# Kernel optimization log

Hardware: AMD Instinct MI355X
Metric: run time of the kernel (lower is better)

## Reference

```python
import jax, jax.numpy as jnp
import numpy as np
from jax import lax

B, C_IN, H, W = 4, 256, 64, 64
C_OUT = 512
KEY_DIM = C_OUT // 2   # 256
VAL_DIM = C_OUT // 2   # 256
HEADS = 8
EPS = 1e-5


def _conv(x, w, stride, pad):
    return lax.conv_general_dilated(
        x, w, (stride, stride), [(pad, pad), (pad, pad)],
        dimension_numbers=('NCHW', 'OIHW', 'NCHW'))


def setup_inputs() -> dict:
    key = jax.random.key(0)
    ks = jax.random.split(key, 10)
    x = jax.random.normal(ks[0], (B, C_IN, H, W), jnp.float32)
    bn_gamma = jax.random.uniform(ks[1], (C_IN,), jnp.float32, 0.5, 1.5)
    bn_beta = jax.random.normal(ks[2], (C_IN,), jnp.float32) * 0.1
    bn_mean = jax.random.normal(ks[3], (C_IN,), jnp.float32) * 0.1
    bn_var = jax.random.uniform(ks[4], (C_IN,), jnp.float32, 0.5, 1.5)
    w_short = jax.random.normal(ks[5], (C_OUT, C_IN, 3, 3), jnp.float32) * (1.0 / np.sqrt(C_IN * 9))
    wq = jax.random.normal(ks[6], (KEY_DIM, C_IN, 1, 1), jnp.float32) * (1.0 / np.sqrt(C_IN))
    wk = jax.random.normal(ks[7], (KEY_DIM, C_IN, 1, 1), jnp.float32) * (1.0 / np.sqrt(C_IN))
    wv = jax.random.normal(ks[8], (VAL_DIM, C_IN, 1, 1), jnp.float32) * (1.0 / np.sqrt(C_IN))
    wo = jax.random.normal(ks[9], (C_OUT, VAL_DIM, 1, 1), jnp.float32) * (1.0 / np.sqrt(VAL_DIM))
    return dict(x=x, bn_gamma=bn_gamma, bn_beta=bn_beta, bn_mean=bn_mean,
                bn_var=bn_var, w_short=w_short, wq=wq, wk=wk, wv=wv, wo=wo)


def reference(x, bn_gamma, bn_beta, bn_mean, bn_var, w_short, wq, wk, wv, wo):
    # BatchNorm (inference: running stats) + ReLU, fused elementwise chain
    inv = bn_gamma / jnp.sqrt(bn_var + EPS)
    h = jax.nn.relu((x - bn_mean[None, :, None, None]) * inv[None, :, None, None]
                    + bn_beta[None, :, None, None])

    # Projection shortcut: 3x3 conv, stride 2, pad 1, no bias -> [B, C_OUT, H/2, W/2]
    shortcut = _conv(h, w_short, 2, 1)

    # DOWN attention: queries at stride 2 (downsampled grid), keys/values at full res
    q = _conv(h, wq, 2, 0)   # [B, KEY_DIM, H/2, W/2]
    k = _conv(h, wk, 1, 0)   # [B, KEY_DIM, H, W]
    v = _conv(h, wv, 1, 0)   # [B, VAL_DIM, H, W]

    Ho, Wo = H // 2, W // 2
    dk = KEY_DIM // HEADS
    dv = VAL_DIM // HEADS
    Nq, Nk = Ho * Wo, H * W

    qh = q.reshape(B, HEADS, dk, Nq)
    kh = k.reshape(B, HEADS, dk, Nk)
    vh = v.reshape(B, HEADS, dv, Nk)

    scale = 1.0 / np.sqrt(dk)
    scores = jnp.einsum('bhdq,bhdk->bhqk', qh, kh) * scale  # [B,H,Nq,Nk]
    attn = jax.nn.softmax(scores, axis=-1)                  # use_softmax=True
    out = jnp.einsum('bhqk,bhdk->bhdq', attn, vh)           # [B,H,dv,Nq]
    out = out.reshape(B, VAL_DIM, Ho, Wo)
    out = _conv(out, wo, 1, 0)                              # [B, C_OUT, Ho, Wo]

    return shortcut + out
```

## Files before the change

### kernel.cpp

```cpp
#include <hip/hip_runtime.h>

#define BB    4
#define CIN   256
#define NPIX  4096
#define COUT  512
#define KD    256
#define HEADS 8
#define NQ    1024
#define NK    4096
#define EPSV  1e-5f
#define QSCALE (0.17677669529663687f * 1.4426950408889634f)

using short8 = __attribute__((ext_vector_type(8))) short;
using f32x4  = __attribute__((ext_vector_type(4))) float;

__device__ __forceinline__ float b2f(unsigned u){ return __uint_as_float(u << 16); }
__device__ __forceinline__ unsigned short f2b(float f){
  unsigned u = __float_as_uint(f);
  return (unsigned short)((u + 0x7fffu + ((u >> 16) & 1u)) >> 16);
}
__device__ __forceinline__ float bnrelu(float xv, float inv, float mu, float bt){
  return fmaxf((xv - mu) * inv + bt, 0.0f);
}
__device__ __forceinline__ unsigned pkbf(float lo, float hi){
  unsigned a = __float_as_uint(lo) + 0x8000u;
  unsigned b = __float_as_uint(hi) + 0x8000u;
  return __builtin_amdgcn_perm(b, a, 0x07060302u);
}
__device__ __forceinline__ unsigned cvtpk(float lo, float hi){
  unsigned r;
  asm("v_cvt_pk_bf16_f32 %0, %1, %2" : "=v"(r) : "v"(lo), "v"(hi));
  return r;
}

__global__ __launch_bounds__(256) void prep_h(
    const float* __restrict__ x, const float* __restrict__ gam,
    const float* __restrict__ bet, const float* __restrict__ mea,
    const float* __restrict__ var, unsigned short* __restrict__ h_t){
  __shared__ unsigned short T[64][264];
  const int b = blockIdx.y;
  const int pix0 = blockIdx.x * 64;
  const int t = threadIdx.x;
  const int w = t >> 6, lane = t & 63;
  for (int cc = 0; cc < 32; ++cc){
    int c0 = cc * 8 + w * 2;
    float i0 = gam[c0]   * rsqrtf(var[c0]   + EPSV), mu0 = mea[c0],   bt0 = bet[c0];
    float i1 = gam[c0+1] * rsqrtf(var[c0+1] + EPSV), mu1 = mea[c0+1], bt1 = bet[c0+1];
    float v0 = bnrelu(x[((size_t)(b*CIN + c0  ))*NPIX + pix0 + lane], i0, mu0, bt0);
    float v1 = bnrelu(x[((size_t)(b*CIN + c0+1))*NPIX + pix0 + lane], i1, mu1, bt1);
    *(unsigned*)&T[lane][c0] = pkbf(v0, v1);
  }
  __syncthreads();
  int p = t >> 2;
  unsigned short* dst = h_t + ((size_t)b * NPIX + pix0 + p) * CIN;
  #pragma unroll
  for (int i = 0; i < 8; ++i){
    int coff = i * 32 + (t & 3) * 8;
    *(uint4*)(dst + coff) = *(const uint4*)&T[p][coff];
  }
}

#define WF_K  2560
#define WF_E  (512*2560)
__global__ __launch_bounds__(256) void prep_w3(
    const float* __restrict__ wsh, const float* __restrict__ wq,
    const float* __restrict__ wk,  const float* __restrict__ wv,
    const float* __restrict__ wo,  unsigned short* __restrict__ W2){
  const int blk = blockIdx.x;
  const int t = threadIdx.x;
  if (blk < 512){
    __shared__ float R[2304];
    const float* src = wsh + (size_t)blk * 2304;
    #pragma unroll
    for (int i = 0; i < 9; ++i) R[i * 256 + t] = src[i * 256 + t];
    __syncthreads();
    unsigned short* dst = W2 + (size_t)blk * WF_K;
    #pragma unroll
    for (int i = 0; i < 9; ++i){
      int kp = i * 256 + t;
      int tap = kp >> 8, ci = kp & 255;
      dst[kp] = f2b(R[ci * 9 + tap]);
    }
  } else if (blk < 704){
    int idx = (blk - 512) * 1024 + t * 4;
    float4 v;
    if (idx < 65536){
      v = *(const float4*)(wq + idx);
      v.x *= QSCALE; v.y *= QSCALE; v.z *= QSCALE; v.w *= QSCALE;
    } else if (idx < 2*65536){ v = *(const float4*)(wk + idx - 65536);
    } else {                   v = *(const float4*)(wv + idx - 2*65536); }
    uint2 pk;
    pk.x = (unsigned)f2b(v.x) | ((unsigned)f2b(v.y) << 16);
    pk.y = (unsigned)f2b(v.z) | ((unsigned)f2b(v.w) << 16);
    *(uint2*)(W2 + WF_E + idx) = pk;
  } else {
    int idx = (blk - 704) * 1024 + t * 4;
    int m = idx >> 8, c = idx & 255;
    float4 v = *(const float4*)(wo + idx);
    uint2 pk;
    pk.x = (unsigned)f2b(v.x) | ((unsigned)f2b(v.y) << 16);
    pk.y = (unsigned)f2b(v.z) | ((unsigned)f2b(v.w) << 16);
    *(uint2*)(W2 + (size_t)m * WF_K + 2304 + c) = pk;
  }
}

__global__ __launch_bounds__(256) void kv_gemm(
    const unsigned short* __restrict__ Wkv,
    const unsigned short* __restrict__ h_t,
    unsigned short* __restrict__ ktg,
    unsigned short* __restrict__ vtg){
  const int b  = blockIdx.z;
  const int m0 = blockIdx.y * 64;
  const bool isv = m0 >= 256;
  const int n0 = blockIdx.x * 128;
  const int t  = threadIdx.x;
  const int w = t >> 6, lane = t & 63, col = lane & 15, quad = lane >> 4;
  const int wm = w & 1, wn = w >> 1;
  __shared__ unsigned short As[64][40];
  __shared__ unsigned short Bs[128][40];
  f32x4 acc[2][4];
  #pragma unroll
  for (int i = 0; i < 2; ++i)
    #pragma unroll
    for (int j = 0; j < 4; ++j) acc[i][j] = (f32x4){0.f,0.f,0.f,0.f};
  const int am = t >> 2, ak = (t & 3) * 8;
  const int bn = t >> 1, bkh = (t & 1) * 16;
  const size_t browbase = ((size_t)b * NPIX + (n0 + bn)) * CIN;

  uint4 av  = *(const uint4*)(Wkv + (size_t)(m0 + am) * 256 + ak);
  uint4 bv0 = *(const uint4*)(h_t + browbase + bkh);
  uint4 bv1 = *(const uint4*)(h_t + browbase + bkh + 8);

  for (int k0 = 0; k0 < 256; k0 += 32){
    *(uint4*)&As[am][ak]      = av;
    *(uint4*)&Bs[bn][bkh]     = bv0;
    *(uint4*)&Bs[bn][bkh + 8] = bv1;
    __syncthreads();
    if (k0 + 32 < 256){
      av  = *(const uint4*)(Wkv + (size_t)(m0 + am) * 256 + k0 + 32 + ak);
      bv0 = *(const uint4*)(h_t + browbase + k0 + 32 + bkh);
      bv1 = *(const uint4*)(h_t + browbase + k0 + 32 + bkh + 8);
    }
    short8 af[2], bf[4];
    af[0] = *(const short8*)&As[wm * 32 +      col][quad * 8];
    af[1] = *(const short8*)&As[wm * 32 + 16 + col][quad * 8];
    #pragma unroll
    for (int j = 0; j < 4; ++j)
      bf[j] = *(const short8*)&Bs[wn * 64 + j * 16 + col][quad * 8];
    if (!isv){
      #pragma unroll
      for (int i = 0; i < 2; ++i)
        #pragma unroll
        for (int j = 0; j < 4; ++j)
          acc[i][j] = __builtin_amdgcn_mfma_f32_16x16x32_bf16(af[i], bf[j], acc[i][j], 0, 0, 0);
    } else {
      #pragma unroll
      for (int i = 0; i < 2; ++i)
        #pragma unroll
        for (int j = 0; j < 4; ++j)
          acc[i][j] = __builtin_amdgcn_mfma_f32_16x16x32_bf16(bf[j], af[i], acc[i][j], 0, 0, 0);
    }
    __syncthreads();
  }

  if (!isv){
    int head = (m0 + wm * 32) >> 5;
    #pragma unroll
    for (int i = 0; i < 2; ++i){
      int d0 = i * 16 + quad * 4;
      #pragma unroll
      for (int j = 0; j < 4; ++j){
        int n = n0 + wn * 64 + j * 16 + col;
        uint2 pk;
        pk.x = pkbf(acc[i][j][0], acc[i][j][1]);
        pk.y = pkbf(acc[i][j][2], acc[i][j][3]);
        *(uint2*)(ktg + ((size_t)(b * HEADS + head) * NK + n) * 32 + d0) = pk;
      }
    }
  } else {
    int head = ((m0 - 256) + wm * 32) >> 5;
    #pragma unroll
    for (int i = 0; i < 2; ++i){
      int d = i * 16 + col;
      #pragma unroll
      for (int j = 0; j < 4; ++j){
        int nb = n0 + wn * 64 + j * 16 + quad * 4;
        size_t addr = (((size_t)(b * HEADS + head) * 128 + (nb >> 5)) * 32 + d) * 32 + (nb & 31);
        uint2 pk;
        pk.x = pkbf(acc[i][j][0], acc[i][j][1]);
        pk.y = pkbf(acc[i][j][2], acc[i][j][3]);
        *(uint2*)(vtg + addr) = pk;
      }
    }
  }
}

__global__ __launch_bounds__(256) void q_gemm(
    const unsigned short* __restrict__ Wq,
    const unsigned short* __restrict__ h_t,
    unsigned short* __restrict__ qt){
  const int b  = blockIdx.z;
  const int m0 = blockIdx.y * 64;
  const int n0 = blockIdx.x * 64;
  const int t  = threadIdx.x;
  const int w = t >> 6, lane = t & 63, col = lane & 15, quad = lane >> 4;
  const int wm = w & 1, wn = w >> 1;
  __shared__ unsigned short As[64][40];
  __shared__ unsigned short Bs[64][40];
  f32x4 acc[2][2];
  #pragma unroll
  for (int i = 0; i < 2; ++i)
    #pragma unroll
    for (int j = 0; j < 2; ++j) acc[i][j] = (f32x4){0.f,0.f,0.f,0.f};
  const int am = t >> 2, ak = (t & 3) * 8;
  const int bn = t >> 2, bk = (t & 3) * 8;
  int n = n0 + bn;
  const size_t browbase = ((size_t)b * NPIX + (((n >> 5) << 7) + ((n & 31) << 1))) * CIN;

  uint4 av = *(const uint4*)(Wq + (size_t)(m0 + am) * 256 + ak);
  uint4 bv = *(const uint4*)(h_t + browbase + bk);

  for (int k0 = 0; k0 < 256; k0 += 32){
    *(uint4*)&As[am][ak] = av;
    *(uint4*)&Bs[bn][bk] = bv;
    __syncthreads();
    if (k0 + 32 < 256){
      av = *(const uint4*)(Wq + (size_t)(m0 + am) * 256 + k0 + 32 + ak);
      bv = *(const uint4*)(h_t + browbase + k0 + 32 + bk);
    }
    short8 af[2], bf[2];
    af[0] = *(const short8*)&As[wm * 32 +      col][quad * 8];
    af[1] = *(const short8*)&As[wm * 32 + 16 + col][quad * 8];
    bf[0] = *(const short8*)&Bs[wn * 32 +      col][quad * 8];
    bf[1] = *(const short8*)&Bs[wn * 32 + 16 + col][quad * 8];
    #pragma unroll
    for (int i = 0; i < 2; ++i)
      #pragma unroll
      for (int j = 0; j < 2; ++j)
        acc[i][j] = __builtin_amdgcn_mfma_f32_16x16x32_bf16(af[i], bf[j], acc[i][j], 0, 0, 0);
    __syncthreads();
  }

  int head = (m0 + wm * 32) >> 5;
  #pragma unroll
  for (int i = 0; i < 2; ++i){
    int d0 = i * 16 + quad * 4;
    #pragma unroll
    for (int j = 0; j < 2; ++j){
      int nn = n0 + wn * 32 + j * 16 + col;
      uint2 pk;
      pk.x = pkbf(acc[i][j][0], acc[i][j][1]);
      pk.y = pkbf(acc[i][j][2], acc[i][j][3]);
      *(uint2*)(qt + ((size_t)(b * HEADS + head) * NQ + nn) * 32 + d0) = pk;
    }
  }
}

__global__ __launch_bounds__(256) void scwo_gemm(
    const unsigned short* __restrict__ Wf,
    const unsigned short* __restrict__ h_t,
    const unsigned short* __restrict__ aot,
    float* __restrict__ outf){
  const int b  = blockIdx.z;
  const int m0 = blockIdx.y * 64;
  const int n0 = blockIdx.x * 64;
  const int t  = threadIdx.x;
  const int w = t >> 6, lane = t & 63, col = lane & 15, quad = lane >> 4;
  const int wm = w & 1, wn = w >> 1;
  __shared__ unsigned short As[64][40];
  __shared__ unsigned short Bs[64][40];
  f32x4 acc[2][2];
  #pragma unroll
  for (int i = 0; i < 2; ++i)
    #pragma unroll
    for (int j = 0; j < 2; ++j) acc[i][j] = (f32x4){0.f,0.f,0.f,0.f};
  const int am = t >> 2, ak = (t & 3) * 8;
  const int bn = t >> 2, bk = (t & 3) * 8;
  const int n = n0 + bn;
  const int oy = n >> 5, ox = n & 31;
  const size_t aobase = ((size_t)b * NQ + n) * KD;

  auto loadB = [&](int k0) -> uint4 {
    if (k0 < 2304){
      int tap = k0 >> 8;
      int ky = tap / 3, kx = tap - ky * 3;
      int iy = 2 * oy + ky - 1, ix = 2 * ox + kx - 1;
      if (((unsigned)iy < 64u) && ((unsigned)ix < 64u))
        return *(const uint4*)(h_t + ((size_t)b * NPIX + iy * 64 + ix) * CIN + (k0 & 255) + bk);
      return make_uint4(0,0,0,0);
    }
    return *(const uint4*)(aot + aobase + (k0 - 2304) + bk);
  };

  uint4 av = *(const uint4*)(Wf + (size_t)(m0 + am) * WF_K + ak);
  uint4 bv = loadB(0);

  for (int k0 = 0; k0 < WF_K; k0 += 32){
    *(uint4*)&As[am][ak] = av;
    *(uint4*)&Bs[bn][bk] = bv;
    __syncthreads();
    if (k0 + 32 < WF_K){
      av = *(const uint4*)(Wf + (size_t)(m0 + am) * WF_K + k0 + 32 + ak);
      bv = loadB(k0 + 32);
    }
    short8 af[2], bf[2];
    af[0] = *(const short8*)&As[wm * 32 +      col][quad * 8];
    af[1] = *(const short8*)&As[wm * 32 + 16 + col][quad * 8];
    bf[0] = *(const short8*)&Bs[wn * 32 +      col][quad * 8];
    bf[1] = *(const short8*)&Bs[wn * 32 + 16 + col][quad * 8];
    #pragma unroll
    for (int i = 0; i < 2; ++i)
      #pragma unroll
      for (int j = 0; j < 2; ++j)
        acc[i][j] = __builtin_amdgcn_mfma_f32_16x16x32_bf16(bf[j], af[i], acc[i][j], 0, 0, 0);
    __syncthreads();
  }

  #pragma unroll
  for (int i = 0; i < 2; ++i){
    int co = m0 + wm * 32 + i * 16 + col;
    #pragma unroll
    for (int j = 0; j < 2; ++j){
      int nb = n0 + wn * 32 + j * 16 + quad * 4;
      float4 o;
      o.x = acc[i][j][0]; o.y = acc[i][j][1];
      o.z = acc[i][j][2]; o.w = acc[i][j][3];
      *(float4*)(outf + ((size_t)(b * COUT + co)) * NQ + nb) = o;
    }
  }
}

__global__ __launch_bounds__(256) void attn8(
    const unsigned short* __restrict__ qt,
    const unsigned short* __restrict__ ktg,
    const unsigned short* __restrict__ vtg,
    unsigned short* __restrict__ aot){
  __shared__ float Om4[4][64][8];
  __shared__ float Ll4[4][64];
  const int bid = blockIdx.x;
  const int xcd = bid & 7, slot = bid >> 3;
  const int bh = xcd * 4 + (slot >> 6);
  const int qblk = slot & 63;
  const int b = bh >> 3, hd = bh & 7;
  const int t = threadIdx.x;
  const int w = t >> 6, lane = t & 63, col = lane & 15, quad = lane >> 4;
  const int q = qblk * 16 + col;

  short8 qf = *(const short8*)(qt + ((size_t)bh * NQ + q) * 32 + quad * 8);
  const unsigned short* kb = ktg + (size_t)bh * NK * 32;
  const unsigned short* vb = vtg + (size_t)bh * 128 * 1024;
  const int ks = w * 1024, ke = ks + 1024;

  short8 kf0 = *(const short8*)(kb + (size_t)(ks +      col) * 32 + quad * 8);
  short8 kf1 = *(const short8*)(kb + (size_t)(ks + 16 + col) * 32 + quad * 8);
  short8 vf0 = *(const short8*)(vb + ((ks >> 5) << 10) +       col * 32 + quad * 8);
  short8 vf1 = *(const short8*)(vb + ((ks >> 5) << 10) + 512 + col * 32 + quad * 8);

  f32x4 O0 = {0.f,0.f,0.f,0.f}, O1 = {0.f,0.f,0.f,0.f}, l4 = {0.f,0.f,0.f,0.f};
  const short8 ones = {0x3F80,0x3F80,0x3F80,0x3F80,0x3F80,0x3F80,0x3F80,0x3F80};

  for (int k0 = ks; k0 < ke; k0 += 32){
    int kn = (k0 + 32 < ke) ? (k0 + 32) : ks;
    int cn = (kn >> 5) << 10;
    short8 nk0 = *(const short8*)(kb + (size_t)(kn +      col) * 32 + quad * 8);
    short8 nk1 = *(const short8*)(kb + (size_t)(kn + 16 + col) * 32 + quad * 8);
    short8 nv0 = *(const short8*)(vb + cn +       col * 32 + quad * 8);
    short8 nv1 = *(const short8*)(vb + cn + 512 + col * 32 + quad * 8);

    f32x4 z = {0.f,0.f,0.f,0.f};
    f32x4 slo = __builtin_amdgcn_mfma_f32_16x16x32_bf16(kf0, qf, z, 0, 0, 0);
    f32x4 shi = __builtin_amdgcn_mfma_f32_16x16x32_bf16(kf1, qf, z, 0, 0, 0);

    unsigned x0 = cvtpk(__builtin_amdgcn_exp2f(slo[0]), __builtin_amdgcn_exp2f(slo[1]));
    unsigned x1 = cvtpk(__builtin_amdgcn_exp2f(slo[2]), __builtin_amdgcn_exp2f(slo[3]));
    unsigned y0 = cvtpk(__builtin_amdgcn_exp2f(shi[0]), __builtin_amdgcn_exp2f(shi[1]));
    unsigned y1 = cvtpk(__builtin_amdgcn_exp2f(shi[2]), __builtin_amdgcn_exp2f(shi[3]));

    asm("v_permlane32_swap_b32 %0, %1" : "+v"(x0), "+v"(y0));
    asm("v_permlane32_swap_b32 %0, %1" : "+v"(x1), "+v"(y1));
    asm("v_permlane16_swap_b32 %0, %1" : "+v"(x0), "+v"(y0));
    asm("v_permlane16_swap_b32 %0, %1" : "+v"(x1), "+v"(y1));
    unsigned f[4] = {x0, x1, y0, y1};
    short8 pf;
    memcpy(&pf, f, 16);

    O0 = __builtin_amdgcn_mfma_f32_16x16x32_bf16(vf0, pf, O0, 0, 0, 0);
    O1 = __builtin_amdgcn_mfma_f32_16x16x32_bf16(vf1, pf, O1, 0, 0, 0);
    l4 = __builtin_amdgcn_mfma_f32_16x16x32_bf16(ones, pf, l4, 0, 0, 0);
    kf0 = nk0; kf1 = nk1; vf0 = nv0; vf1 = nv1;
  }

  Ll4[w][lane] = l4[0];
  *(f32x4*)&Om4[w][lane][0] = O0;
  *(f32x4*)&Om4[w][lane][4] = O1;
  __syncthreads();
  if (w == 0){
    float L = l4[0] + Ll4[1][lane] + Ll4[2][lane] + Ll4[3][lane];
    float o[8];
    #pragma unroll
    for (int j = 0; j < 8; ++j)
      o[j] = Om4[0][lane][j] + Om4[1][lane][j] + Om4[2][lane][j] + Om4[3][lane][j];
    float inv = 1.0f / L;
    unsigned short* dst = aot + ((size_t)(b * NQ + q)) * KD + hd * 32;
    uint2 pk;
    pk.x = pkbf(o[0] * inv, o[1] * inv);
    pk.y = pkbf(o[2] * inv, o[3] * inv);
    *(uint2*)(dst + quad * 4) = pk;
    pk.x = pkbf(o[4] * inv, o[5] * inv);
    pk.y = pkbf(o[6] * inv, o[7] * inv);
    *(uint2*)(dst + 16 + quad * 4) = pk;
  }
}

extern "C" void kernel_launch(void* const* d_in, const int* in_sizes, int n_in,
                              void* d_out, int out_size, void* d_ws, size_t ws_size,
                              hipStream_t stream){
  const float* x   = (const float*)d_in[0];
  const float* bg  = (const float*)d_in[1];
  const float* bbt = (const float*)d_in[2];
  const float* bm  = (const float*)d_in[3];
  const float* bv  = (const float*)d_in[4];
  const float* wsh = (const float*)d_in[5];
  const float* wq  = (const float*)d_in[6];
  const float* wk  = (const float*)d_in[7];
  const float* wvv = (const float*)d_in[8];
  const float* wo  = (const float*)d_in[9];
  float* out = (float*)d_out;

  unsigned short* h_t = (unsigned short*)d_ws;
  unsigned short* W2  = h_t + (size_t)BB * NPIX * CIN;
  unsigned short* qt  = W2  + (WF_E + 3*65536);
  unsigned short* aot = qt  + (size_t)BB * HEADS * NQ * 32;
  unsigned short* ktg = aot + (size_t)BB * NQ * KD;
  unsigned short* vtg = ktg + (size_t)BB * HEADS * NK * 32;
  size_t need = ((size_t)(vtg + (size_t)BB * HEADS * 32 * NK - h_t)) * 2;
  if (ws_size < need) return;

  unsigned short* Wf   = W2;
  unsigned short* wq2  = W2 + WF_E;
  unsigned short* wkv2 = wq2 + 65536;

  prep_h<<<dim3(64, 4), dim3(256), 0, stream>>>(x, bg, bbt, bm, bv, h_t);
  prep_w3<<<dim3(832), dim3(256), 0, stream>>>(wsh, wq, wk, wvv, wo, W2);
  q_gemm<<<dim3(16, 4, 4), dim3(256), 0, stream>>>(wq2, h_t, qt);
  kv_gemm<<<dim3(32, 8, 4), dim3(256), 0, stream>>>(wkv2, h_t, ktg, vtg);
  attn8<<<dim3(2048), dim3(256), 0, stream>>>(qt, ktg, vtg, aot);
  scwo_gemm<<<dim3(16, 8, 4), dim3(256), 0, stream>>>(Wf, h_t, aot, out);
}
```

Baseline: 205.3 us.

## Share K/V tiles across query blocks via double-buffered LDS in attention

The attention kernel changes from four waves splitting the key range for one 16-query block, with an LDS reduction at the end, to eight waves each owning a different 16-query block. All eight waves iterate over the full key range, and K/V tiles are staged cooperatively into double-buffered shared memory. This cuts redundant global/L2 reads of K and V by sharing each tile across eight query blocks and removes the final cross-wave reduction. In exchange there is a block-wide barrier every iteration, only 256 blocks (one per CU), and a longer serial key loop per wave.

```diff
diff --git a/kernel.cpp b/kernel.cpp
--- a/kernel.cpp
+++ b/kernel.cpp
@@ -330,86 +330,88 @@
   }
 }
 
-__global__ __launch_bounds__(256) void attn8(
+__global__ __launch_bounds__(512) void attn9b(
     const unsigned short* __restrict__ qt,
     const unsigned short* __restrict__ ktg,
     const unsigned short* __restrict__ vtg,
     unsigned short* __restrict__ aot){
-  __shared__ float Om4[4][64][8];
-  __shared__ float Ll4[4][64];
+  __shared__ unsigned short KV[2][4096];
   const int bid = blockIdx.x;
-  const int xcd = bid & 7, slot = bid >> 3;
-  const int bh = xcd * 4 + (slot >> 6);
-  const int qblk = slot & 63;
+  const int xcd = bid & 7, idx = bid >> 3;
+  const int bh = xcd * 4 + (idx & 3);
+  const int qg = idx >> 2;
   const int b = bh >> 3, hd = bh & 7;
   const int t = threadIdx.x;
   const int w = t >> 6, lane = t & 63, col = lane & 15, quad = lane >> 4;
-  const int q = qblk * 16 + col;
+  const int q = (qg * 8 + w) * 16 + col;
 
   short8 qf = *(const short8*)(qt + ((size_t)bh * NQ + q) * 32 + quad * 8);
   const unsigned short* kb = ktg + (size_t)bh * NK * 32;
   const unsigned short* vb = vtg + (size_t)bh * 128 * 1024;
-  const int ks = w * 1024, ke = ks + 1024;
-
-  short8 kf0 = *(const short8*)(kb + (size_t)(ks +      col) * 32 + quad * 8);
-  short8 kf1 = *(const short8*)(kb + (size_t)(ks + 16 + col) * 32 + quad * 8);
-  short8 vf0 = *(const short8*)(vb + ((ks >> 5) << 10) +       col * 32 + quad * 8);
-  short8 vf1 = *(const short8*)(vb + ((ks >> 5) << 10) + 512 + col * 32 + quad * 8);
+
+  const int sg = (w & 3) >> 1, sf = w & 1;
+  const size_t ksrc = (size_t)(32 * sg + 16 * sf + col) * 32 + quad * 8;
+  const size_t vsrc = (size_t)sg * 1024 + (size_t)(16 * sf + col) * 32 + quad * 8;
+  unsigned short* dstp = &KV[0][w * 512 + lane * 8];
 
   f32x4 O0 = {0.f,0.f,0.f,0.f}, O1 = {0.f,0.f,0.f,0.f}, l4 = {0.f,0.f,0.f,0.f};
   const short8 ones = {0x3F80,0x3F80,0x3F80,0x3F80,0x3F80,0x3F80,0x3F80,0x3F80};
 
-  for (int k0 = ks; k0 < ke; k0 += 32){
-    int kn = (k0 + 32 < ke) ? (k0 + 32) : ks;
-    int cn = (kn >> 5) << 10;
-    short8 nk0 = *(const short8*)(kb + (size_t)(kn +      col) * 32 + quad * 8);
-    short8 nk1 = *(const short8*)(kb + (size_t)(kn + 16 + col) * 32 + quad * 8);
-    short8 nv0 = *(const short8*)(vb + cn +       col * 32 + quad * 8);
-    short8 nv1 = *(const short8*)(vb + cn + 512 + col * 32 + quad * 8);
-
-    f32x4 z = {0.f,0.f,0.f,0.f};
-    f32x4 slo = __builtin_amdgcn_mfma_f32_16x16x32_bf16(kf0, qf, z, 0, 0, 0);
-    f32x4 shi = __builtin_amdgcn_mfma_f32_16x16x32_bf16(kf1, qf, z, 0, 0, 0);
-
-    unsigned x0 = cvtpk(__builtin_amdgcn_exp2f(slo[0]), __builtin_amdgcn_exp2f(slo[1]));
-    unsigned x1 = cvtpk(__builtin_amdgcn_exp2f(slo[2]), __builtin_amdgcn_exp2f(slo[3]));
-    unsigned y0 = cvtpk(__builtin_amdgcn_exp2f(shi[0]), __builtin_amdgcn_exp2f(shi[1]));
-    unsigned y1 = cvtpk(__builtin_amdgcn_exp2f(shi[2]), __builtin_amdgcn_exp2f(shi[3]));
-
-    asm("v_permlane32_swap_b32 %0, %1" : "+v"(x0), "+v"(y0));
-    asm("v_permlane32_swap_b32 %0, %1" : "+v"(x1), "+v"(y1));
-    asm("v_permlane16_swap_b32 %0, %1" : "+v"(x0), "+v"(y0));
-    asm("v_permlane16_swap_b32 %0, %1" : "+v"(x1), "+v"(y1));
-    unsigned f[4] = {x0, x1, y0, y1};
-    short8 pf;
-    memcpy(&pf, f, 16);
-
-    O0 = __builtin_amdgcn_mfma_f32_16x16x32_bf16(vf0, pf, O0, 0, 0, 0);
-    O1 = __builtin_amdgcn_mfma_f32_16x16x32_bf16(vf1, pf, O1, 0, 0, 0);
-    l4 = __builtin_amdgcn_mfma_f32_16x16x32_bf16(ones, pf, l4, 0, 0, 0);
-    kf0 = nk0; kf1 = nk1; vf0 = nv0; vf1 = nv1;
-  }
-
-  Ll4[w][lane] = l4[0];
-  *(f32x4*)&Om4[w][lane][0] = O0;
-  *(f32x4*)&Om4[w][lane][4] = O1;
+  uint4 stg = (w < 4) ? *(const uint4*)(kb + ksrc)
+                      : *(const uint4*)(vb + vsrc);
+  *(uint4*)dstp = stg;
   __syncthreads();
-  if (w == 0){
-    float L = l4[0] + Ll4[1][lane] + Ll4[2][lane] + Ll4[3][lane];
-    float o[8];
-    #pragma unroll
-    for (int j = 0; j < 8; ++j)
-      o[j] = Om4[0][lane][j] + Om4[1][lane][j] + Om4[2][lane][j] + Om4[3][lane][j];
-    float inv = 1.0f / L;
-    unsigned short* dst = aot + ((size_t)(b * NQ + q)) * KD + hd * 32;
-    uint2 pk;
-    pk.x = pkbf(o[0] * inv, o[1] * inv);
-    pk.y = pkbf(o[2] * inv, o[3] * inv);
-    *(uint2*)(dst + quad * 4) = pk;
-    pk.x = pkbf(o[4] * inv, o[5] * inv);
-    pk.y = pkbf(o[6] * inv, o[7] * inv);
-    *(uint2*)(dst + 16 + quad * 4) = pk;
-  }
+
+  for (int s = 0; s < 64; ++s){
+    const int cur = s & 1;
+    uint4 nxt;
+    if (s + 1 < 64){
+      size_t soff = (size_t)(s + 1) * 2048;
+      nxt = (w < 4) ? *(const uint4*)(kb + soff + ksrc)
+                    : *(const uint4*)(vb + soff + vsrc);
+    }
+    #pragma unroll
+    for (int g = 0; g < 2; ++g){
+      const unsigned short* Kp = &KV[cur][g * 1024];
+      short8 kf0 = *(const short8*)(Kp +       lane * 8);
+      short8 kf1 = *(const short8*)(Kp + 512 + lane * 8);
+      f32x4 z = {0.f,0.f,0.f,0.f};
+      f32x4 slo = __builtin_amdgcn_mfma_f32_16x16x32_bf16(kf0, qf, z, 0, 0, 0);
+      f32x4 shi = __builtin_amdgcn_mfma_f32_16x16x32_bf16(kf1, qf, z, 0, 0, 0);
+
+      unsigned x0 = cvtpk(__builtin_amdgcn_exp2f(slo[0]), __builtin_amdgcn_exp2f(slo[1]));
+      unsigned x1 = cvtpk(__builtin_amdgcn_exp2f(slo[2]), __builtin_amdgcn_exp2f(slo[3]));
+      unsigned y0 = cvtpk(__builtin_amdgcn_exp2f(shi[0]), __builtin_amdgcn_exp2f(shi[1]));
+      unsigned y1 = cvtpk(__builtin_amdgcn_exp2f(shi[2]), __builtin_amdgcn_exp2f(shi[3]));
+      asm("v_permlane32_swap_b32 %0, %1" : "+v"(x0), "+v"(y0));
+      asm("v_permlane32_swap_b32 %0, %1" : "+v"(x1), "+v"(y1));
+      asm("v_permlane16_swap_b32 %0, %1" : "+v"(x0), "+v"(y0));
+      asm("v_permlane16_swap_b32 %0, %1" : "+v"(x1), "+v"(y1));
+      unsigned f[4] = {x0, x1, y0, y1};
+      short8 pf;
+      memcpy(&pf, f, 16);
+
+      const unsigned short* Vp = &KV[cur][2048 + g * 1024];
+      short8 vf0 = *(const short8*)(Vp +       lane * 8);
+      short8 vf1 = *(const short8*)(Vp + 512 + lane * 8);
+      O0 = __builtin_amdgcn_mfma_f32_16x16x32_bf16(vf0, pf, O0, 0, 0, 0);
+      O1 = __builtin_amdgcn_mfma_f32_16x16x32_bf16(vf1, pf, O1, 0, 0, 0);
+      l4 = __builtin_amdgcn_mfma_f32_16x16x32_bf16(ones, pf, l4, 0, 0, 0);
+    }
+    if (s + 1 < 64)
+      *(uint4*)(dstp + (size_t)(cur ^ 1) * 4096) = nxt;
+    __syncthreads();
+  }
+
+  float inv = 1.0f / l4[0];
+  unsigned short* dst = aot + ((size_t)(b * NQ + q)) * KD + hd * 32;
+  uint2 pk;
+  pk.x = pkbf(O0[0] * inv, O0[1] * inv);
+  pk.y = pkbf(O0[2] * inv, O0[3] * inv);
+  *(uint2*)(dst + quad * 4) = pk;
+  pk.x = pkbf(O1[0] * inv, O1[1] * inv);
+  pk.y = pkbf(O1[2] * inv, O1[3] * inv);
+  *(uint2*)(dst + 16 + quad * 4) = pk;
 }
 
 extern "C" void kernel_launch(void* const* d_in, const int* in_sizes, int n_in,
@@ -444,6 +446,6 @@
   prep_w3<<<dim3(832), dim3(256), 0, stream>>>(wsh, wq, wk, wvv, wo, W2);
   q_gemm<<<dim3(16, 4, 4), dim3(256), 0, stream>>>(wq2, h_t, qt);
   kv_gemm<<<dim3(32, 8, 4), dim3(256), 0, stream>>>(wkv2, h_t, ktg, vtg);
-  attn8<<<dim3(2048), dim3(256), 0, stream>>>(qt, ktg, vtg, aot);
+  attn9b<<<dim3(256), dim3(512), 0, stream>>>(qt, ktg, vtg, aot);
   scwo_gemm<<<dim3(16, 8, 4), dim3(256), 0, stream>>>(Wf, h_t, aot, out);
 }
```

Result: faster. 175.6 us (-14.4%).
